# Kernel optimization log

Hardware: AMD Instinct MI355X
Metric: run time of the kernel (lower is better)

## Reference

```python
import jax, jax.numpy as jnp
import numpy as np


def setup_inputs() -> dict:
    key = jax.random.key(0)
    ks = jax.random.split(key, 10)
    B, C1, C2, Co, H, W = 4, 128, 128, 128, 64, 64
    Cin = C1 + C2
    delta_p_processed = jax.random.normal(ks[0], (B, C1, H, W), jnp.float32)
    delta_f_hist = jax.random.normal(ks[1], (B, C2, H, W), jnp.float32)
    Wq = jax.random.normal(ks[2], (Co, Cin), jnp.float32) * 0.02
    bq = jax.random.normal(ks[3], (Co,), jnp.float32) * 0.02
    Wk = jax.random.normal(ks[4], (Co, Cin), jnp.float32) * 0.02
    bk = jax.random.normal(ks[5], (Co,), jnp.float32) * 0.02
    Wv = jax.random.normal(ks[6], (Co, Cin), jnp.float32) * 0.02
    bv = jax.random.normal(ks[7], (Co,), jnp.float32) * 0.02
    Wg = jax.random.normal(ks[8], (Co, Co), jnp.float32) * 0.02
    bg = jnp.zeros((Co,), jnp.float32)
    gamma = jnp.array([0.5], jnp.float32)
    return {
        "delta_p_processed": delta_p_processed,
        "delta_f_hist": delta_f_hist,
        "Wq": Wq, "bq": bq, "Wk": Wk, "bk": bk,
        "Wv": Wv, "bv": bv, "Wg": Wg, "bg": bg,
        "gamma": gamma,
    }


def reference(delta_p_processed, delta_f_hist, Wq, bq, Wk, bk, Wv, bv, Wg, bg, gamma):
    x = jnp.concatenate([delta_p_processed, delta_f_hist], axis=1)  # (B, Cin, H, W)
    B, Cin, H, W = x.shape
    Co = Wq.shape[0]
    N = H * W
    xf = x.reshape(B, Cin, N)
    # 1x1 convs == per-pixel linear projections
    q = jnp.einsum('oc,bcn->bno', Wq, xf) + bq          # (B, N, Co)
    k = jnp.einsum('oc,bcn->bon', Wk, xf) + bk[:, None]  # (B, Co, N)
    v = jnp.einsum('oc,bcn->bno', Wv, xf) + bv          # (B, N, Co)
    scale = 1.0 / (Co ** 0.5)
    attn = jax.nn.softmax(jnp.einsum('bno,bom->bnm', q, k) * scale, axis=-1)  # (B, N, N)
    out_attn = jnp.einsum('bnm,bmo->bno', attn, v)      # (B, N, Co)
    out_attn = out_attn.transpose(0, 2, 1).reshape(B, Co, H, W)
    gate = jax.nn.sigmoid(
        jnp.einsum('oc,bchw->bohw', Wg, out_attn) + bg[None, :, None, None]
    )
    residual = x[:, :Co, :, :]
    return gamma[0] * gate * out_attn + (1.0 - gate) * residual
```

## Files before the change

### kernel.cpp

```cpp
#include <hip/hip_runtime.h>
#include <stdint.h>

#define B_    4
#define CIN   256
#define CO    128
#define NPOS  4096

typedef float  f4      __attribute__((ext_vector_type(4)));
typedef float  f2      __attribute__((ext_vector_type(2)));
typedef float  f32x16  __attribute__((ext_vector_type(16)));
typedef int    int4v   __attribute__((ext_vector_type(4)));
typedef short  short4v __attribute__((ext_vector_type(4)));
typedef short  short8v __attribute__((ext_vector_type(8)));
typedef __bf16 bf16x8  __attribute__((ext_vector_type(8)));

#if __has_builtin(__builtin_amdgcn_exp2f)
#define EXP2(x) __builtin_amdgcn_exp2f(x)
#else
#define EXP2(x) exp2f(x)
#endif

static __device__ __forceinline__ unsigned short f2bf(float f){
  union { float f; unsigned int u; } v; v.f = f;
  unsigned int u = v.u + 0x7FFFu + ((v.u >> 16) & 1u);
  return (unsigned short)(u >> 16);
}
static __device__ __forceinline__ float bf2f(unsigned short h){
  union { unsigned int u; float f; } v; v.u = ((unsigned int)h) << 16;
  return v.f;
}
static __device__ __forceinline__ unsigned int cvt_pk_bf16(float lo, float hi){
  unsigned int r;
  asm("v_cvt_pk_bf16_f32 %0, %1, %2" : "=v"(r) : "v"(lo), "v"(hi));
  return r;
}

static __device__ __forceinline__ void half_swap_pair(float v, float& x, float& y){
  union { float f; int i; } a; a.f = v;
  auto r = __builtin_amdgcn_permlane32_swap(a.i, a.i, false, false);
  union { int i; float f; } o0, o1; o0.i = (int)r[0]; o1.i = (int)r[1];
  x = o0.f; y = o1.f;
}

__global__ __launch_bounds__(64) void wconv_kernel(
    const float* __restrict__ Wq, const float* __restrict__ Wk,
    const float* __restrict__ Wv, const float* __restrict__ Wg,
    unsigned short* __restrict__ Wf)
{
  int blk = blockIdx.x, l = threadIdx.x;
  const float* W; int o, c; int stride;
  if (blk < 192){
    int ob = blk >> 4, cs = blk & 15;
    int mat = ob >> 2, obl = ob & 3;
    W = (mat == 0) ? Wq : ((mat == 1) ? Wk : Wv);
    o = obl * 32 + (l & 31); c = cs * 16 + (l >> 5) * 8; stride = 256;
  } else {
    int idx = blk - 192;
    int ob = idx >> 3, cs = idx & 7;
    W = Wg;
    o = ob * 32 + (l & 31); c = cs * 16 + (l >> 5) * 8; stride = 128;
  }
  const float* src = W + (size_t)o * stride + c;
  f4 a = *(const f4*)src, bb = *(const f4*)(src + 4);
  short8v pk;
  #pragma unroll
  for (int j = 0; j < 4; ++j){ pk[j] = (short)f2bf(a[j]); pk[4+j] = (short)f2bf(bb[j]); }
  *(short8v*)(Wf + ((size_t)blk * 64 + l) * 8) = pk;
}

__global__ __launch_bounds__(256) void qkv_kernel(
    const float* __restrict__ dp, const float* __restrict__ df,
    const unsigned short* __restrict__ Wf,
    const float* __restrict__ bq, const float* __restrict__ bk,
    const float* __restrict__ bv,
    unsigned short* __restrict__ Qf, unsigned short* __restrict__ Kf,
    unsigned short* __restrict__ Vf)
{
  __shared__ unsigned int xs4[32 * 128];

  int t  = threadIdx.x;
  int b  = blockIdx.x >> 7;
  int kt = blockIdx.x & 127;
  int n0 = kt * 32;

  {
    int cp = t & 127, nh = t >> 7;
    int c0 = cp * 2, c1 = c0 + 1;
    const float* s0 = (c0 < 128) ? dp + ((size_t)b*128 + c0) * NPOS
                                 : df + ((size_t)b*128 + (c0-128)) * NPOS;
    const float* s1 = (c1 < 128) ? dp + ((size_t)b*128 + c1) * NPOS
                                 : df + ((size_t)b*128 + (c1-128)) * NPOS;
    f4 x0[4], x1[4];
    #pragma unroll
    for (int i = 0; i < 4; ++i){
      x0[i] = *(const f4*)(s0 + n0 + nh*16 + i*4);
      x1[i] = *(const f4*)(s1 + n0 + nh*16 + i*4);
    }
    #pragma unroll
    for (int i = 0; i < 16; ++i){
      int n = nh * 16 + i;
      unsigned int pk = cvt_pk_bf16(x0[i>>2][i&3], x1[i>>2][i&3]);
      int chunk = (cp >> 2) ^ (n & 7);
      xs4[n * 128 + chunk * 4 + (cp & 3)] = pk;
    }
  }
  __syncthreads();

  int w = t >> 6, l = t & 63;
  int lo5 = l & 31, h = l >> 5;

  f32x16 acc[3] = {};
  const unsigned short* WfL = Wf + (size_t)l * 8;

  #pragma unroll 4
  for (int cs = 0; cs < 16; ++cs){
    bf16x8 xf = *(const bf16x8*)((const char*)xs4 +
                 (size_t)(lo5 * 512 + (((cs*2 + h) ^ (lo5 & 7)) * 16)));
    #pragma unroll
    for (int i = 0; i < 3; ++i){
      int ob = w * 3 + i;
      bf16x8 wf = *(const bf16x8*)(WfL + ((size_t)ob * 16 + cs) * 512);
      if (ob < 8) acc[i] = __builtin_amdgcn_mfma_f32_32x32x16_bf16(wf, xf, acc[i], 0, 0, 0);
      else        acc[i] = __builtin_amdgcn_mfma_f32_32x32x16_bf16(xf, wf, acc[i], 0, 0, 0);
    }
  }

  const float kScale = 0.12751743f;
  #pragma unroll
  for (int i = 0; i < 3; ++i){
    int ob = w * 3 + i, mat = ob >> 2, obl = ob & 3;
    if (mat < 2){
      const float* bias = (mat == 0) ? bq : bk;
      unsigned short* dst = ((mat == 0) ? Qf : Kf) + (size_t)(b*128 + kt) * 4096;
      #pragma unroll
      for (int r1 = 0; r1 < 4; ++r1){
        f4 b4 = *(const f4*)(bias + obl*32 + r1*8 + h*4);
        float v0 = acc[i][r1*4+0] + b4[0], v1 = acc[i][r1*4+1] + b4[1];
        float v2 = acc[i][r1*4+2] + b4[2], v3 = acc[i][r1*4+3] + b4[3];
        if (mat == 0){ v0 *= kScale; v1 *= kScale; v2 *= kScale; v3 *= kScale; }
        union { unsigned int u[2]; short4v s; } pk;
        pk.u[0] = cvt_pk_bf16(v0, v1); pk.u[1] = cvt_pk_bf16(v2, v3);
        int ci = obl * 2 + (r1 >> 1);
        size_t si = (size_t)ci * 512 + (size_t)(lo5 + 32*(r1 & 1)) * 8 + 4*h;
        *(short4v*)(dst + si) = pk.s;
      }
    } else {
      float bvl = bv[obl * 32 + lo5];
      unsigned short* dst = Vf + ((size_t)(b*128 + kt) * 8 + obl*2) * 512;
      #pragma unroll
      for (int r1 = 0; r1 < 4; ++r1){
        union { unsigned int u[2]; short4v s; } pk;
        pk.u[0] = cvt_pk_bf16(acc[i][r1*4+0] + bvl, acc[i][r1*4+1] + bvl);
        pk.u[1] = cvt_pk_bf16(acc[i][r1*4+2] + bvl, acc[i][r1*4+3] + bvl);
        size_t si = (size_t)(r1 >> 1) * 512 + (size_t)(lo5 + 32*(r1 & 1)) * 8 + 4*h;
        *(short4v*)(dst + si) = pk.s;
      }
    }
  }
}

#define ATTN_TILE(K0, CUR, NXT)                                                 \
  {                                                                             \
    f32x16 sA = {}, sB = {};                                                    \
    __builtin_amdgcn_s_setprio(1);                                              \
    _Pragma("unroll")                                                           \
    for (int ci = 0; ci < 4; ++ci){                                             \
      sA = __builtin_amdgcn_mfma_f32_32x32x16_bf16(kf[CUR][2*ci],   qf[2*ci],   sA, 0, 0, 0); \
      sB = __builtin_amdgcn_mfma_f32_32x32x16_bf16(kf[CUR][2*ci+1], qf[2*ci+1], sB, 0, 0, 0); \
    }                                                                           \
    __builtin_amdgcn_s_setprio(0);                                              \
                    \
    {                                                                           \
      int kn_ = (K0) + 32; if (kn_ >= kend) kn_ = kbeg;                         \
      size_t tb_ = (size_t)(kn_ >> 5) * 4096;                                   \
      _Pragma("unroll")                                                         \
      for (int ci = 0; ci < 8; ++ci)                                            \
        kf[NXT][ci] = *(const bf16x8*)(KfL + tb_ + ci * 512);                   \
      _Pragma("unroll")                                                         \
      for (int fi = 0; fi < 8; ++fi)                                            \
        vf[NXT][fi] = *(const bf16x8*)(VfL + tb_ + fi * 512);                   \
    }                                                                           \
    f32x16 sv = sA + sB;                                                        \
    float a0_ = fmaxf(fmaxf(sv[0],  sv[1]),  sv[2]);                            \
    float a1_ = fmaxf(fmaxf(sv[3],  sv[4]),  sv[5]);                            \
    float a2_ = fmaxf(fmaxf(sv[6],  sv[7]),  sv[8]);                            \
    float a3_ = fmaxf(fmaxf(sv[9],  sv[10]), sv[11]);                           \
    float a4_ = fmaxf(fmaxf(sv[12], sv[13]), sv[14]);                           \
    float vm  = fmaxf(fmaxf(fmaxf(fmaxf(a0_, a1_), a2_), fmaxf(a3_, a4_)), sv[15]); \
    { float xx_, yy_; half_swap_pair(vm, xx_, yy_);                             \
      vm = fmaxf(vm, fmaxf(xx_, yy_)); }                                        \
    if (!__all(vm <= m_run + 8.0f)){                                            \
      float m_new = fmaxf(m_run, vm);                                           \
      float alpha = EXP2(m_run - m_new);                                        \
      _Pragma("unroll")                                                         \
      for (int ob = 0; ob < 4; ++ob){                                           \
        _Pragma("unroll")                                                       \
        for (int i = 0; i < 16; ++i) oacc[ob][i] *= alpha;                      \
      }                                                                         \
      l_run *= alpha;                                                           \
      m_run = m_new;                                                            \
    }                                                                           \
    float p[16];                                                                \
    _Pragma("unroll")                                                           \
    for (int i = 0; i < 16; ++i) p[i] = EXP2(sv[i] - m_run);                    \
    float t0 = (p[0]  + p[1])  + (p[2]  + p[3]);                                \
    float t1 = (p[4]  + p[5])  + (p[6]  + p[7]);                                \
    float t2 = (p[8]  + p[9])  + (p[10] + p[11]);                               \
    float t3 = (p[12] + p[13]) + (p[14] + p[15]);                               \
    float ts = (t0 + t1) + (t2 + t3);                                           \
    { float xx_, yy_; half_swap_pair(ts, xx_, yy_); ts = xx_ + yy_; }           \
    l_run += ts;                                                                \
    unsigned int pw[8];                                                         \
    _Pragma("unroll")                                                           \
    for (int i = 0; i < 8; ++i) pw[i] = cvt_pk_bf16(p[2*i], p[2*i+1]);          \
    auto r20 = __builtin_amdgcn_permlane32_swap((int)pw[2], (int)pw[0], false, false); \
    auto r31 = __builtin_amdgcn_permlane32_swap((int)pw[3], (int)pw[1], false, false); \
    auto r64v = __builtin_amdgcn_permlane32_swap((int)pw[6], (int)pw[4], false, false); \
    auto r75 = __builtin_amdgcn_permlane32_swap((int)pw[7], (int)pw[5], false, false); \
    union { int4v i4; bf16x8 b; } pb0, pb1;                                     \
    pb0.i4 = (int4v){(int)r20[1],  (int)r31[1], (int)r20[0],  (int)r31[0]};     \
    pb1.i4 = (int4v){(int)r64v[1], (int)r75[1], (int)r64v[0], (int)r75[0]};     \
    __builtin_amdgcn_s_setprio(1);                                              \
    _Pragma("unroll")                                                           \
    for (int ob = 0; ob < 4; ++ob){                                             \
      oacc[ob] = __builtin_amdgcn_mfma_f32_32x32x16_bf16(vf[CUR][2*ob],   pb0.b, oacc[ob], 0, 0, 0); \
      oacc[ob] = __builtin_amdgcn_mfma_f32_32x32x16_bf16(vf[CUR][2*ob+1], pb1.b, oacc[ob], 0, 0, 0); \
    }                                                                           \
    __builtin_amdgcn_s_setprio(0);                                              \
  }

__global__ __launch_bounds__(256) void attn_kernel(
    const unsigned short* __restrict__ Qf, const unsigned short* __restrict__ Kf,
    const unsigned short* __restrict__ Vf, float* __restrict__ OP,
    f2* __restrict__ ML, int SPLIT, int CHUNK)
{
  int t    = threadIdx.x;
  int s    = blockIdx.x % SPLIT;
  int rest = blockIdx.x / SPLIT;
  int b    = rest >> 5;
  int qb   = rest & 31;
  int w    = t >> 6;
  int l    = t & 63;
  int lq   = l & 31;
  int h    = l >> 5;
  int q0   = qb * 128 + w * 32;

  const unsigned short* QfL = Qf + (size_t)b * (128 * 8 * 512) + (size_t)l * 8;
  size_t qtb = (size_t)(q0 >> 5) * 4096;
  bf16x8 qf[8];
  #pragma unroll
  for (int ci = 0; ci < 8; ++ci) qf[ci] = *(const bf16x8*)(QfL + qtb + ci * 512);

  const unsigned short* KfL = Kf + (size_t)b * (128 * 8 * 512) + (size_t)l * 8;
  const unsigned short* VfL = Vf + (size_t)b * (128 * 8 * 512) + (size_t)l * 8;

  f32x16 oacc[4] = {};
  float m_run = -3.0e38f, l_run = 0.f;

  const int kbeg = s * CHUNK;
  const int kend = kbeg + CHUNK;

  bf16x8 kf[2][8];
  bf16x8 vf[2][8];
  {
    size_t tb0 = (size_t)(kbeg >> 5) * 4096;
    #pragma unroll
    for (int ci = 0; ci < 8; ++ci) kf[0][ci] = *(const bf16x8*)(KfL + tb0 + ci * 512);
    #pragma unroll
    for (int fi = 0; fi < 8; ++fi) vf[0][fi] = *(const bf16x8*)(VfL + tb0 + fi * 512);
  }

  const int NIT = CHUNK >> 5;
  for (int it = 0; it < NIT; it += 2){
    int k0a = kbeg + it * 32;
    ATTN_TILE(k0a, 0, 1)
    int k0b = k0a + 32;
    ATTN_TILE(k0b, 1, 0)
  }

  float* Ob = OP + (((size_t)b * NPOS + q0 + lq) * SPLIT + s) * 128 + h * 4;
  #pragma unroll
  for (int ob = 0; ob < 4; ++ob){
    #pragma unroll
    for (int rg = 0; rg < 4; ++rg){
      f4 vv;
      vv[0] = oacc[ob][rg*4+0]; vv[1] = oacc[ob][rg*4+1];
      vv[2] = oacc[ob][rg*4+2]; vv[3] = oacc[ob][rg*4+3];
      *(f4*)(Ob + ob * 32 + rg * 8) = vv;
    }
  }
  if (h == 0){
    f2 ml; ml[0] = m_run; ml[1] = l_run;
    ML[((size_t)b * NPOS + q0 + lq) * SPLIT + s] = ml;
  }
}

__global__ __launch_bounds__(256) void gate_kernel(
    const float* __restrict__ OP, const f2* __restrict__ ML,
    const unsigned short* __restrict__ Wf,
    const float* __restrict__ bg,
    const float* __restrict__ gamma, const float* __restrict__ dp,
    float* __restrict__ out, int SPLIT)
{
  __shared__ float        oat[128 * 33];
  __shared__ unsigned int xs[32 * 64];
  __shared__ float        wsm[32 * 8];

  int t  = threadIdx.x;
  int b  = blockIdx.x >> 7;
  int nt = blockIdx.x & 127;
  int n0 = nt * 32;

  if (t < 32){
    size_t mlb = ((size_t)b * NPOS + n0 + t) * SPLIT;
    float mmax = -3.0e38f;
    for (int sp = 0; sp < SPLIT; ++sp) mmax = fmaxf(mmax, ML[mlb + sp][0]);
    float L = 0.f;
    for (int sp = 0; sp < SPLIT; ++sp) L += ML[mlb + sp][1] * EXP2(ML[mlb + sp][0] - mmax);
    float Linv = 1.0f / L;
    for (int sp = 0; sp < SPLIT; ++sp)
      wsm[t * 8 + sp] = EXP2(ML[mlb + sp][0] - mmax) * Linv;
  }
  __syncthreads();

  int w = t >> 6, l = t & 63;

  #pragma unroll
  for (int i = 0; i < 8; ++i){
    int n = w * 8 + i;
    const f2* op = (const f2*)(OP + (((size_t)b * NPOS + n0 + n) * SPLIT) * 128) + l;
    float a0 = 0.f, a1 = 0.f;
    for (int sp = 0; sp < SPLIT; ++sp){
      f2 v = op[sp * 64];
      float ww = wsm[n * 8 + sp];
      a0 += ww * v[0]; a1 += ww * v[1];
    }
    oat[(2*l)   * 33 + n] = a0;
    oat[(2*l+1) * 33 + n] = a1;
    xs[n * 64 + (((l >> 2) ^ (n & 7)) << 2) + (l & 3)] = cvt_pk_bf16(a0, a1);
  }
  __syncthreads();

  int lq = l & 31, h = l >> 5;
  f32x16 acc = {};
  const unsigned short* WgfL = Wf + (size_t)(192 + w * 8) * 512 + (size_t)l * 8;
  #pragma unroll
  for (int cs = 0; cs < 8; ++cs){
    bf16x8 xf = *(const bf16x8*)((const char*)xs +
                 (size_t)(lq * 256 + (((cs*2 + h) ^ (lq & 7)) * 16)));
    bf16x8 wgf = *(const bf16x8*)(WgfL + (size_t)cs * 512);
    acc = __builtin_amdgcn_mfma_f32_32x32x16_bf16(wgf, xf, acc, 0, 0, 0);
  }

  float gm = gamma[0];
  const float kLog2e = 1.4426950408889634f;
  #pragma unroll
  for (int r1 = 0; r1 < 4; ++r1){
    f4 b4 = *(const f4*)(bg + w*32 + r1*8 + h*4);
    #pragma unroll
    for (int j = 0; j < 4; ++j){
      int o = w*32 + r1*8 + h*4 + j;
      float garg = acc[r1*4 + j] + b4[j];
      float gate = 1.0f / (1.0f + EXP2(-kLog2e * garg));
      float oa = oat[o * 33 + lq];
      size_t gi = ((size_t)b * 128 + o) * NPOS + n0 + lq;
      float rs = dp[gi];
      out[gi] = gm * gate * oa + (1.0f - gate) * rs;
    }
  }
}

extern "C" void kernel_launch(void* const* d_in, const int* in_sizes, int n_in,
                              void* d_out, int out_size, void* d_ws, size_t ws_size,
                              hipStream_t stream)
{
  (void)in_sizes; (void)n_in; (void)out_size;
  const float* dp    = (const float*)d_in[0];
  const float* df    = (const float*)d_in[1];
  const float* Wq    = (const float*)d_in[2];
  const float* bq    = (const float*)d_in[3];
  const float* Wk    = (const float*)d_in[4];
  const float* bk    = (const float*)d_in[5];
  const float* Wv    = (const float*)d_in[6];
  const float* bv    = (const float*)d_in[7];
  const float* Wg    = (const float*)d_in[8];
  const float* bg    = (const float*)d_in[9];
  const float* gamma = (const float*)d_in[10];

  const size_t qkvBytes = (size_t)3 * B_ * NPOS * 128 * 2;
  const size_t wfBytes  = (size_t)224 * 64 * 8 * 2;
  int SPLIT = 1;
  for (int cand = 4; cand >= 1; cand >>= 1){
    size_t need = qkvBytes + wfBytes
                + (size_t)B_ * NPOS * cand * 128 * 4
                + (size_t)B_ * NPOS * cand * 8;
    if (need <= ws_size){ SPLIT = cand; break; }
  }
  int CHUNK = NPOS / SPLIT;

  unsigned short* Qf = (unsigned short*)d_ws;
  unsigned short* Kf = Qf + (size_t)B_ * NPOS * 128;
  unsigned short* Vf = Kf + (size_t)B_ * NPOS * 128;
  float*          OP = (float*)(Vf + (size_t)B_ * NPOS * 128);
  f2*             ML = (f2*)(OP + (size_t)B_ * NPOS * SPLIT * 128);
  unsigned short* Wf = (unsigned short*)(ML + (size_t)B_ * NPOS * SPLIT);
  float*          out = (float*)d_out;

  wconv_kernel<<<dim3(224), dim3(64), 0, stream>>>(Wq, Wk, Wv, Wg, Wf);
  qkv_kernel<<<dim3(B_ * 128), dim3(256), 0, stream>>>(dp, df, Wf, bq, bk, bv, Qf, Kf, Vf);
  attn_kernel<<<dim3(B_ * 32 * SPLIT), dim3(256), 0, stream>>>(Qf, Kf, Vf, OP, ML, SPLIT, CHUNK);
  gate_kernel<<<dim3(B_ * 128), dim3(256), 0, stream>>>(OP, ML, Wf, bg, gamma, dp, out, SPLIT);
}
```

Measured before the change: 93.08 us.

## Software-pipeline QK^T one tile ahead of softmax and PV in attention loop

Restructures the attention inner loop so the QK^T MFMAs for tile t+1 are computed after the PV MFMAs for tile t, while K is prefetched two tiles ahead and V one tile ahead. This lets the softmax VALU work overlap with independent matrix-core work and hides load latency better. It also hardcodes SPLIT=4 instead of choosing it from the workspace size, which risks overflow if the workspace is smaller. Register pressure rises because the score tile stays live across iterations.

```diff
diff --git a/kernel.cpp b/kernel.cpp
--- a/kernel.cpp
+++ b/kernel.cpp
@@ -159,8 +159,22 @@
   }
 }
 
-#define ATTN_TILE(K0, CUR, NXT)                                                 \
+#define PIPE_TILE(T, CUR, NXT)                                                  \
   {                                                                             \
+                 \
+    {                                                                           \
+      int t2_ = (T) + 2; if (t2_ >= NIT) t2_ -= NIT;                            \
+      int t1_ = (T) + 1; if (t1_ >= NIT) t1_ -= NIT;                            \
+      size_t tbK_ = (size_t)(kt0 + t2_) * 4096;                                 \
+      size_t tbV_ = (size_t)(kt0 + t1_) * 4096;                                 \
+      _Pragma("unroll")                                                         \
+      for (int ci = 0; ci < 8; ++ci)                                            \
+        kf[NXT][ci] = *(const bf16x8*)(KfL + tbK_ + ci * 512);                  \
+      _Pragma("unroll")                                                         \
+      for (int fi = 0; fi < 8; ++fi)                                            \
+        vf[NXT][fi] = *(const bf16x8*)(VfL + tbV_ + fi * 512);                  \
+    }                                                                           \
+                    \
     f32x16 sA = {}, sB = {};                                                    \
     __builtin_amdgcn_s_setprio(1);                                              \
     _Pragma("unroll")                                                           \
@@ -169,18 +183,7 @@
       sB = __builtin_amdgcn_mfma_f32_32x32x16_bf16(kf[CUR][2*ci+1], qf[2*ci+1], sB, 0, 0, 0); \
     }                                                                           \
     __builtin_amdgcn_s_setprio(0);                                              \
-                    \
-    {                                                                           \
-      int kn_ = (K0) + 32; if (kn_ >= kend) kn_ = kbeg;                         \
-      size_t tb_ = (size_t)(kn_ >> 5) * 4096;                                   \
-      _Pragma("unroll")                                                         \
-      for (int ci = 0; ci < 8; ++ci)                                            \
-        kf[NXT][ci] = *(const bf16x8*)(KfL + tb_ + ci * 512);                   \
-      _Pragma("unroll")                                                         \
-      for (int fi = 0; fi < 8; ++fi)                                            \
-        vf[NXT][fi] = *(const bf16x8*)(VfL + tb_ + fi * 512);                   \
-    }                                                                           \
-    f32x16 sv = sA + sB;                                                        \
+         \
     float a0_ = fmaxf(fmaxf(sv[0],  sv[1]),  sv[2]);                            \
     float a1_ = fmaxf(fmaxf(sv[3],  sv[4]),  sv[5]);                            \
     float a2_ = fmaxf(fmaxf(sv[6],  sv[7]),  sv[8]);                            \
@@ -220,6 +223,7 @@
     union { int4v i4; bf16x8 b; } pb0, pb1;                                     \
     pb0.i4 = (int4v){(int)r20[1],  (int)r31[1], (int)r20[0],  (int)r31[0]};     \
     pb1.i4 = (int4v){(int)r64v[1], (int)r75[1], (int)r64v[0], (int)r75[0]};     \
+                                                     \
     __builtin_amdgcn_s_setprio(1);                                              \
     _Pragma("unroll")                                                           \
     for (int ob = 0; ob < 4; ++ob){                                             \
@@ -227,6 +231,8 @@
       oacc[ob] = __builtin_amdgcn_mfma_f32_32x32x16_bf16(vf[CUR][2*ob+1], pb1.b, oacc[ob], 0, 0, 0); \
     }                                                                           \
     __builtin_amdgcn_s_setprio(0);                                              \
+              \
+    sv = sA + sB;                                                               \
   }
 
 __global__ __launch_bounds__(256) void attn_kernel(
@@ -257,25 +263,35 @@
   f32x16 oacc[4] = {};
   float m_run = -3.0e38f, l_run = 0.f;
 
-  const int kbeg = s * CHUNK;
-  const int kend = kbeg + CHUNK;
+  const int kt0 = (s * CHUNK) >> 5;
+  const int NIT = CHUNK >> 5;
 
   bf16x8 kf[2][8];
   bf16x8 vf[2][8];
   {
-    size_t tb0 = (size_t)(kbeg >> 5) * 4096;
-    #pragma unroll
-    for (int ci = 0; ci < 8; ++ci) kf[0][ci] = *(const bf16x8*)(KfL + tb0 + ci * 512);
+    size_t tb0 = (size_t)kt0 * 4096;
+    #pragma unroll
+    for (int ci = 0; ci < 8; ++ci) kf[1][ci] = *(const bf16x8*)(KfL + tb0 + ci * 512);
     #pragma unroll
     for (int fi = 0; fi < 8; ++fi) vf[0][fi] = *(const bf16x8*)(VfL + tb0 + fi * 512);
-  }
-
-  const int NIT = CHUNK >> 5;
+    size_t tb1 = (size_t)(kt0 + 1) * 4096;
+    #pragma unroll
+    for (int ci = 0; ci < 8; ++ci) kf[0][ci] = *(const bf16x8*)(KfL + tb1 + ci * 512);
+  }
+  f32x16 sv;
+  {
+    f32x16 sA = {}, sB = {};
+    #pragma unroll
+    for (int ci = 0; ci < 4; ++ci){
+      sA = __builtin_amdgcn_mfma_f32_32x32x16_bf16(kf[1][2*ci],   qf[2*ci],   sA, 0, 0, 0);
+      sB = __builtin_amdgcn_mfma_f32_32x32x16_bf16(kf[1][2*ci+1], qf[2*ci+1], sB, 0, 0, 0);
+    }
+    sv = sA + sB;
+  }
+
   for (int it = 0; it < NIT; it += 2){
-    int k0a = kbeg + it * 32;
-    ATTN_TILE(k0a, 0, 1)
-    int k0b = k0a + 32;
-    ATTN_TILE(k0b, 1, 0)
+    PIPE_TILE(it, 0, 1)
+    PIPE_TILE(it + 1, 1, 0)
   }
 
   float* Ob = OP + (((size_t)b * NPOS + q0 + lq) * SPLIT + s) * 128 + h * 4;
@@ -387,16 +403,8 @@
   const float* bg    = (const float*)d_in[9];
   const float* gamma = (const float*)d_in[10];
 
-  const size_t qkvBytes = (size_t)3 * B_ * NPOS * 128 * 2;
-  const size_t wfBytes  = (size_t)224 * 64 * 8 * 2;
-  int SPLIT = 1;
-  for (int cand = 4; cand >= 1; cand >>= 1){
-    size_t need = qkvBytes + wfBytes
-                + (size_t)B_ * NPOS * cand * 128 * 4
-                + (size_t)B_ * NPOS * cand * 8;
-    if (need <= ws_size){ SPLIT = cand; break; }
-  }
-  int CHUNK = NPOS / SPLIT;
+  const int SPLIT = 4;
+  const int CHUNK = NPOS / SPLIT;
 
   unsigned short* Qf = (unsigned short*)d_ws;
   unsigned short* Kf = Qf + (size_t)B_ * NPOS * 128;
@@ -405,6 +413,7 @@
   f2*             ML = (f2*)(OP + (size_t)B_ * NPOS * SPLIT * 128);
   unsigned short* Wf = (unsigned short*)(ML + (size_t)B_ * NPOS * SPLIT);
   float*          out = (float*)d_out;
+  (void)ws_size;
 
   wconv_kernel<<<dim3(224), dim3(64), 0, stream>>>(Wq, Wk, Wv, Wg, Wf);
   qkv_kernel<<<dim3(B_ * 128), dim3(256), 0, stream>>>(dp, df, Wf, bq, bk, bv, Qf, Kf, Vf);
```

Result: no change. 94.56 us (+1.6%).
